# Optimization experiments

Hardware: AMD Instinct MI355X
Metric: run time of the kernel (lower is better)

Reference implementation:

```python
import jax, jax.numpy as jnp
import numpy as np

N_NODES = 100000
N_EDGES = 3200000


def setup_inputs() -> dict:
    key = jax.random.key(0)
    k = jax.random.split(key, 6)
    x = jax.random.normal(k[0], (N_NODES, 3), dtype=jnp.float32)
    edge_index = jax.random.randint(k[1], (2, N_EDGES), 0, N_NODES, dtype=jnp.int64)
    # Glorot-ish init for the two GCNConv layers (3->16, 16->7), bias=True (PyG default)
    W1 = jax.random.normal(k[2], (3, 16), dtype=jnp.float32) * (1.0 / np.sqrt(3.0))
    b1 = jnp.zeros((16,), dtype=jnp.float32)
    W2 = jax.random.normal(k[3], (16, 7), dtype=jnp.float32) * (1.0 / np.sqrt(16.0))
    b2 = jnp.zeros((7,), dtype=jnp.float32)
    return {"x": x, "edge_index": edge_index, "W1": W1, "b1": b1, "W2": W2, "b2": b2}


def _gcn_conv(x, W, b, src, dst, norm, n_nodes):
    # x: [N, Fin]; src/dst/norm: [E+N] (self-loops appended); out: [N, Fout]
    h = x @ W                                   # small GEMM
    msg = h[src] * norm[:, None]                # gather + scale per edge
    out = jax.ops.segment_sum(msg, dst, num_segments=n_nodes)  # scatter-add
    return out + b


def reference(x, edge_index, W1, b1, W2, b2):
    n = x.shape[0]
    loop = jnp.arange(n, dtype=edge_index.dtype)
    src = jnp.concatenate([edge_index[0], loop])
    dst = jnp.concatenate([edge_index[1], loop])
    # symmetric normalization D^-1/2 (A+I) D^-1/2, deg counted at targets
    deg = jax.ops.segment_sum(jnp.ones(src.shape[0], dtype=x.dtype), dst, num_segments=n)
    dinv = jnp.where(deg > 0, jax.lax.rsqrt(deg), 0.0)
    norm = dinv[src] * dinv[dst]                # [E+N]

    h = _gcn_conv(x, W1, b1, src, dst, norm, n)
    h = jax.nn.relu(h)
    h = _gcn_conv(h, W2, b2, src, dst, norm, n)
    return jax.nn.log_softmax(h, axis=1)
```

## Files before the change

### kernel.cpp

```cpp
#include <hip/hip_runtime.h>
#include <hip/hip_fp16.h>
#include <math.h>

#define N_NODES 100000
#define N_EDGES 3200000
#define NB 512
#define NPB 196
#define CAP 7168
#define EPB 16384
#define NBLK ((N_EDGES + EPB - 1) / EPB)

#define FSCALE 1048576.0f
#define INV_FSCALE (1.0f / 1048576.0f)


__device__ inline float2 h2f2(unsigned int u) {
    __half2 h = *reinterpret_cast<__half2*>(&u);
    return make_float2(__low2float(h), __high2float(h));
}

__device__ inline int fx(float v) { return __float2int_rn(v * FSCALE); }

__global__ void k_zero(int* __restrict__ gcur) {
    int i = blockIdx.x * blockDim.x + threadIdx.x;
    if (i < NB) gcur[i] = 0;
}

__global__ void __launch_bounds__(1024) k_bucket(
        const int* __restrict__ ei, int* __restrict__ gcur,
        unsigned int* __restrict__ bdata) {
    __shared__ int cnt[NB];
    __shared__ int gb[NB];
    int blk = blockIdx.x, tid = threadIdx.x;
    int e0 = blk * EPB;
    int ecnt = min(EPB, N_EDGES - e0);
    const int* dst = ei + N_EDGES + e0;
    const int* src = ei + e0;

    if (tid < NB) cnt[tid] = 0;
    __syncthreads();
    for (int i = tid; i < ecnt; i += 1024) atomicAdd(&cnt[dst[i] / NPB], 1);
    __syncthreads();
    if (tid < NB) {
        int c = cnt[tid];
        gb[tid] = (c > 0) ? atomicAdd(&gcur[tid], c) : 0;
        cnt[tid] = 0;
    }
    __syncthreads();
    for (int i = tid; i < ecnt; i += 1024) {
        int d = dst[i];
        int b = d / NPB;
        int dl = d - b * NPB;
        int pos = atomicAdd(&cnt[b], 1) + gb[b];
        if (pos < CAP)
            bdata[(size_t)b * CAP + pos] = ((unsigned)dl << 17) | (unsigned)src[i];
    }
}

__global__ void k_deg(const int* __restrict__ gcur, const unsigned int* __restrict__ bdata,
                      const float* __restrict__ x, __half2* __restrict__ xh) {
    __shared__ int cnt[NPB];
    int b = blockIdx.x, t = threadIdx.x;
    for (int j = t; j < NPB; j += 512) cnt[j] = 0;
    __syncthreads();
    int n = min(gcur[b], CAP);
    const unsigned int* p = bdata + (size_t)b * CAP;
    for (int e = t; e < n; e += 512) atomicAdd(&cnt[p[e] >> 17], 1);
    __syncthreads();
    int base = b * NPB;
    for (int j = t; j < NPB; j += 512) {
        int i = base + j;
        if (i < N_NODES) {
            float di = rsqrtf((float)cnt[j] + 1.0f);
            xh[2 * i + 0] = __floats2half2_rn(di * x[3 * i + 0], di * x[3 * i + 1]);
            xh[2 * i + 1] = __floats2half2_rn(di * x[3 * i + 2], di);
        }
    }
}

__global__ void __launch_bounds__(1024) k_l1(
        const int* __restrict__ gcur, const unsigned int* __restrict__ bdata,
        const __half2* __restrict__ xh, const float* __restrict__ W1,
        const float* __restrict__ b1, const float* __restrict__ W2,
        uint4* __restrict__ th) {
    __shared__ int a[NPB * 3];
    int b = blockIdx.x, tid = threadIdx.x;
    for (int j = tid; j < NPB * 3; j += 1024) a[j] = 0;
    __syncthreads();
    int n = min(gcur[b], CAP);
    const unsigned int* p = bdata + (size_t)b * CAP;
    const uint2* xg = (const uint2*)xh;
    for (int e = tid; e < n; e += 2048) {
        unsigned int pk0 = p[e];
        int e1 = e + 1024;
        unsigned int pk1 = (e1 < n) ? p[e1] : 0u;
        uint2 g0 = xg[pk0 & 0x1FFFF];
        int dl0 = pk0 >> 17;
        float2 f01 = h2f2(g0.x);
        float2 f2w = h2f2(g0.y);
        atomicAdd(&a[dl0 * 3 + 0], fx(f01.x));
        atomicAdd(&a[dl0 * 3 + 1], fx(f01.y));
        atomicAdd(&a[dl0 * 3 + 2], fx(f2w.x));
        if (e1 < n) {
            uint2 g1 = xg[pk1 & 0x1FFFF];
            int dl1 = pk1 >> 17;
            float2 q01 = h2f2(g1.x);
            float2 q2w = h2f2(g1.y);
            atomicAdd(&a[dl1 * 3 + 0], fx(q01.x));
            atomicAdd(&a[dl1 * 3 + 1], fx(q01.y));
            atomicAdd(&a[dl1 * 3 + 2], fx(q2w.x));
        }
    }
    __syncthreads();
    int base = b * NPB;
    for (int j = tid; j < NPB; j += 1024) {
        int i = base + j;
        if (i >= N_NODES) continue;
        uint2 gi = xg[i];
        float2 f01 = h2f2(gi.x);
        float2 f2w = h2f2(gi.y);
        float di = f2w.y;
        float a0 = di * ((float)a[j * 3 + 0] * INV_FSCALE + f01.x);
        float a1 = di * ((float)a[j * 3 + 1] * INV_FSCALE + f01.y);
        float a2 = di * ((float)a[j * 3 + 2] * INV_FSCALE + f2w.x);
        float r[16];
#pragma unroll
        for (int k = 0; k < 16; ++k)
            r[k] = fmaxf(a0 * W1[k] + a1 * W1[16 + k] + a2 * W1[32 + k] + b1[k], 0.0f);
        float t[7];
#pragma unroll
        for (int c = 0; c < 7; ++c) {
            float v = 0.0f;
#pragma unroll
            for (int k = 0; k < 16; ++k) v += r[k] * W2[7 * k + c];
            t[c] = di * v;
        }
        __half2 h0 = __floats2half2_rn(t[0], t[1]);
        __half2 h1 = __floats2half2_rn(t[2], t[3]);
        __half2 h2 = __floats2half2_rn(t[4], t[5]);
        __half2 h3 = __floats2half2_rn(t[6], di);
        uint4 pk;
        pk.x = *reinterpret_cast<unsigned int*>(&h0);
        pk.y = *reinterpret_cast<unsigned int*>(&h1);
        pk.z = *reinterpret_cast<unsigned int*>(&h2);
        pk.w = *reinterpret_cast<unsigned int*>(&h3);
        th[i] = pk;
    }
}

__global__ void __launch_bounds__(1024) k_l2(
        const int* __restrict__ gcur, const unsigned int* __restrict__ bdata,
        const uint4* __restrict__ th, const float* __restrict__ b2,
        float* __restrict__ out) {
    __shared__ int a[NPB * 7];
    int b = blockIdx.x, tid = threadIdx.x;
    for (int j = tid; j < NPB * 7; j += 1024) a[j] = 0;
    __syncthreads();
    int n = min(gcur[b], CAP);
    const unsigned int* p = bdata + (size_t)b * CAP;
    for (int e = tid; e < n; e += 2048) {
        unsigned int pk0 = p[e];
        int e1 = e + 1024;
        unsigned int pk1 = (e1 < n) ? p[e1] : 0u;
        uint4 g0 = th[pk0 & 0x1FFFF];
        int dl0 = pk0 >> 17;
        float2 u0 = h2f2(g0.x), u1 = h2f2(g0.y), u2 = h2f2(g0.z), u3 = h2f2(g0.w);
        atomicAdd(&a[dl0 * 7 + 0], fx(u0.x));
        atomicAdd(&a[dl0 * 7 + 1], fx(u0.y));
        atomicAdd(&a[dl0 * 7 + 2], fx(u1.x));
        atomicAdd(&a[dl0 * 7 + 3], fx(u1.y));
        atomicAdd(&a[dl0 * 7 + 4], fx(u2.x));
        atomicAdd(&a[dl0 * 7 + 5], fx(u2.y));
        atomicAdd(&a[dl0 * 7 + 6], fx(u3.x));
        if (e1 < n) {
            uint4 g1 = th[pk1 & 0x1FFFF];
            int dl1 = pk1 >> 17;
            float2 v0 = h2f2(g1.x), v1 = h2f2(g1.y), v2 = h2f2(g1.z), v3 = h2f2(g1.w);
            atomicAdd(&a[dl1 * 7 + 0], fx(v0.x));
            atomicAdd(&a[dl1 * 7 + 1], fx(v0.y));
            atomicAdd(&a[dl1 * 7 + 2], fx(v1.x));
            atomicAdd(&a[dl1 * 7 + 3], fx(v1.y));
            atomicAdd(&a[dl1 * 7 + 4], fx(v2.x));
            atomicAdd(&a[dl1 * 7 + 5], fx(v2.y));
            atomicAdd(&a[dl1 * 7 + 6], fx(v3.x));
        }
    }
    __syncthreads();
    int base = b * NPB;
    for (int j = tid; j < NPB; j += 1024) {
        int i = base + j;
        if (i >= N_NODES) continue;
        uint4 gi = th[i];
        float2 t0 = h2f2(gi.x), t1 = h2f2(gi.y), t2 = h2f2(gi.z), t3 = h2f2(gi.w);
        float di = t3.y;
        float thv[7] = {t0.x, t0.y, t1.x, t1.y, t2.x, t2.y, t3.x};
        float v[7];
        float m = -1e30f;
#pragma unroll
        for (int c = 0; c < 7; ++c) {
            v[c] = di * ((float)a[j * 7 + c] * INV_FSCALE + thv[c]) + b2[c];
            m = fmaxf(m, v[c]);
        }
        float sum = 0.0f;
#pragma unroll
        for (int c = 0; c < 7; ++c) sum += expf(v[c] - m);
        float lse = m + logf(sum);
#pragma unroll
        for (int c = 0; c < 7; ++c) out[7 * i + c] = v[c] - lse;
    }
}

extern "C" void kernel_launch(void* const* d_in, const int* in_sizes, int n_in,
                              void* d_out, int out_size, void* d_ws, size_t ws_size,
                              hipStream_t stream) {
    const float* x  = (const float*)d_in[0];
    const int*   ei = (const int*)d_in[1];
    const float* W1 = (const float*)d_in[2];
    const float* b1 = (const float*)d_in[3];
    const float* W2 = (const float*)d_in[4];
    const float* b2 = (const float*)d_in[5];
    float* out = (float*)d_out;

    char* ws = (char*)d_ws;
    int*          gcur  = (int*)ws;          ws += 4096;
    __half2*      xh    = (__half2*)ws;      ws += (size_t)N_NODES * 8;
    uint4*        th    = (uint4*)ws;        ws += (size_t)N_NODES * 16;
    unsigned int* bdata = (unsigned int*)ws;

    k_zero<<<2, 256, 0, stream>>>(gcur);
    k_bucket<<<NBLK, 1024, 0, stream>>>(ei, gcur, bdata);
    k_deg<<<NB, 512, 0, stream>>>(gcur, bdata, x, xh);
    k_l1<<<NB, 1024, 0, stream>>>(gcur, bdata, xh, W1, b1, W2, th);
    k_l2<<<NB, 1024, 0, stream>>>(gcur, bdata, th, b2, out);
}
```

Measured before the change: 79.42 us.

## Use fewer larger buckets and register-cached vectorized edge bucketing

Reduces bucket count from 512 to 128 with larger node ranges per bucket and capacity scaled accordingly. The bucketing kernel now has each thread load 16 contiguous edges via int4 vector loads, keep bucket ids and packed payloads in registers, and reuse them for the scatter pass instead of re-reading the edge arrays. This aims to cut global read traffic and atomic bin pressure in bucketing. The tradeoff is that the gather/aggregation kernels launch only 128 blocks, which may underuse the GPU's compute units and increase per-block serial work.

```diff
diff --git a/kernel.cpp b/kernel.cpp
--- a/kernel.cpp
+++ b/kernel.cpp
@@ -4,10 +4,10 @@
 
 #define N_NODES 100000
 #define N_EDGES 3200000
-#define NB 512
-#define NPB 196
-#define CAP 7168
-#define EPB 16384
+#define NB 128
+#define NPB 784
+#define CAP 27136
+#define EPB 8192
 #define NBLK ((N_EDGES + EPB - 1) / EPB)
 
 #define FSCALE 1048576.0f
@@ -26,11 +26,12 @@
     if (i < NB) gcur[i] = 0;
 }
 
-__global__ void __launch_bounds__(1024) k_bucket(
+__global__ void __launch_bounds__(512) k_bucket(
         const int* __restrict__ ei, int* __restrict__ gcur,
         unsigned int* __restrict__ bdata) {
     __shared__ int cnt[NB];
     __shared__ int gb[NB];
+    __shared__ int cur[NB];
     int blk = blockIdx.x, tid = threadIdx.x;
     int e0 = blk * EPB;
     int ecnt = min(EPB, N_EDGES - e0);
@@ -39,21 +40,58 @@
 
     if (tid < NB) cnt[tid] = 0;
     __syncthreads();
-    for (int i = tid; i < ecnt; i += 1024) atomicAdd(&cnt[dst[i] / NPB], 1);
+
+    int base = tid * 16;
+    int mine = (base < ecnt) ? min(16, ecnt - base) : 0;
+    unsigned int pay[16];
+    int bk[16];
+
+    if (mine == 16) {
+        int4 d4[4], s4[4];
+#pragma unroll
+        for (int g = 0; g < 4; ++g) d4[g] = ((const int4*)(dst + base))[g];
+#pragma unroll
+        for (int g = 0; g < 4; ++g) s4[g] = ((const int4*)(src + base))[g];
+        const int* dd = (const int*)d4;
+        const int* ss = (const int*)s4;
+#pragma unroll
+        for (int j = 0; j < 16; ++j) {
+            int d = dd[j];
+            int b = d / NPB;
+            int dl = d - b * NPB;
+            bk[j] = b;
+            pay[j] = ((unsigned)dl << 17) | (unsigned)ss[j];
+            atomicAdd(&cnt[b], 1);
+        }
+    } else if (mine > 0) {
+#pragma unroll
+        for (int j = 0; j < 16; ++j) {
+            if (j < mine) {
+                int d = dst[base + j];
+                int b = d / NPB;
+                int dl = d - b * NPB;
+                bk[j] = b;
+                pay[j] = ((unsigned)dl << 17) | (unsigned)src[base + j];
+                atomicAdd(&cnt[b], 1);
+            } else {
+                bk[j] = 0; pay[j] = 0;
+            }
+        }
+    }
     __syncthreads();
     if (tid < NB) {
         int c = cnt[tid];
         gb[tid] = (c > 0) ? atomicAdd(&gcur[tid], c) : 0;
-        cnt[tid] = 0;
-    }
-    __syncthreads();
-    for (int i = tid; i < ecnt; i += 1024) {
-        int d = dst[i];
-        int b = d / NPB;
-        int dl = d - b * NPB;
-        int pos = atomicAdd(&cnt[b], 1) + gb[b];
-        if (pos < CAP)
-            bdata[(size_t)b * CAP + pos] = ((unsigned)dl << 17) | (unsigned)src[i];
+        cur[tid] = 0;
+    }
+    __syncthreads();
+#pragma unroll
+    for (int j = 0; j < 16; ++j) {
+        if (j < mine) {
+            int b = bk[j];
+            int pos = atomicAdd(&cur[b], 1) + gb[b];
+            if (pos < CAP) bdata[(size_t)b * CAP + pos] = pay[j];
+        }
     }
 }
 
@@ -227,8 +265,8 @@
     uint4*        th    = (uint4*)ws;        ws += (size_t)N_NODES * 16;
     unsigned int* bdata = (unsigned int*)ws;
 
-    k_zero<<<2, 256, 0, stream>>>(gcur);
-    k_bucket<<<NBLK, 1024, 0, stream>>>(ei, gcur, bdata);
+    k_zero<<<1, 256, 0, stream>>>(gcur);
+    k_bucket<<<NBLK, 512, 0, stream>>>(ei, gcur, bdata);
     k_deg<<<NB, 512, 0, stream>>>(gcur, bdata, x, xh);
     k_l1<<<NB, 1024, 0, stream>>>(gcur, bdata, xh, W1, b1, W2, th);
     k_l2<<<NB, 1024, 0, stream>>>(gcur, bdata, th, b2, out);
```

Measured after the change: 95.22 us. 19.9% more time.
